# Kernel optimization log

Hardware: AMD Instinct MI355X
Metric: run time of the kernel (lower is better)

## Reference

```python
import jax, jax.numpy as jnp
import numpy as np

B, T, D = 2, 2048, 2048
N, KH, H = 16, 8, 128  # query heads, kv heads, head_dim
S = 2048               # cache size
EPS = 1e-6
ROPE_THETA = 1000000.0
K_MASK = -0.7 * float(np.finfo(np.float32).max)  # jax _get_large_negative(float32)


def _rms_norm(x, w):
    rms = jnp.sqrt(jnp.mean(x.astype(jnp.float32) ** 2, axis=-1, keepdims=True) + EPS)
    return (w * x / rms).astype(x.dtype)


def _rope_embeddings(positions, head_dim):
    fraction = jnp.arange(0, head_dim, 2, dtype=jnp.float32) / head_dim
    inv_freq = 1.0 / (ROPE_THETA ** fraction)
    sinusoid = jnp.einsum('BT,k->BTk', positions.astype(jnp.float32), inv_freq,
                          precision=jax.lax.Precision.HIGHEST)
    return jnp.sin(sinusoid), jnp.cos(sinusoid)


def _apply_rope(x, sin, cos):
    h = x.shape[-1] // 2
    x1, x2 = x[..., :h], x[..., h:]
    s, c = sin[:, :, None, :], cos[:, :, None, :]
    return jnp.concatenate([x1 * c - x2 * s, x2 * c + x1 * s], axis=-1).astype(x.dtype)


def _positions_from_segment_ids(seg):
    t = seg.shape[1]
    pos = jnp.arange(t, dtype=jnp.int32)[None, :] - jnp.argmax(seg, axis=1)[:, None]
    return jnp.where(seg != 0, pos, 2 ** 30)


def _num_left_pad(seg):
    return jnp.sum(jnp.cumsum(seg != 0, axis=-1) == 0, axis=-1).astype(jnp.int32)


def _attention(x, q_w, k_w, v_w, o_w, q_norm_w, k_norm_w, k_cache, v_cache,
               segment_ids, start_ind, cur_ind):
    b, t, _ = x.shape
    s = k_cache.shape[1]
    n, kh, h = q_w.shape[1], k_w.shape[1], q_w.shape[2]

    q = _rms_norm(jnp.einsum('BTD,DNH->BTNH', x, q_w), q_norm_w)  # [B,T,N,H]
    k = _rms_norm(jnp.einsum('BSD,DKH->BSKH', x, k_w), k_norm_w)  # [B,T,K,H]
    v = jnp.einsum('BSD,DKH->BSKH', x, v_w)                       # [B,T,K,H]

    start = jnp.where(start_ind < 0, _num_left_pad(segment_ids), start_ind)
    pos = _positions_from_segment_ids(segment_ids) + cur_ind
    sin, cos = _rope_embeddings(pos, h)
    q = _apply_rope(q, sin, cos)
    k = _apply_rope(k, sin, cos)

    # KV-cache update at cur_ind
    k_cache = jax.lax.dynamic_update_slice(k_cache, k, (0, cur_ind, 0, 0))
    v_cache = jax.lax.dynamic_update_slice(v_cache, v, (0, cur_ind, 0, 0))

    # GQA: group query heads per kv head
    qg = q.reshape(b, t, kh, n // kh, h)
    logits = jnp.einsum('BTHGD,BSHD->BHGTS', qg, k_cache) * (h ** -0.5)

    q_pos = cur_ind + jnp.arange(t, dtype=jnp.int32)[None, :] - start[:, None]  # [B,T]
    ts = jnp.arange(s, dtype=jnp.int32)
    kv_seg = (ts[None, :] >= start[:, None]) & (ts[None, :] < cur_ind + t)      # [B,S] bool
    k_pos = ts[None, :] - start[:, None]                                        # [B,S]
    causal = k_pos[:, None, :] <= q_pos[:, :, None]                             # [B,T,S]
    # faithful to original: bool kv segment ids compared against int segment_ids
    seg_mask = kv_seg[:, None, :].astype(segment_ids.dtype) == segment_ids[:, :, None]
    final_mask = (causal & seg_mask)[:, None, None, :, :]                       # [B,1,1,T,S]

    logits = jnp.where(final_mask, logits, K_MASK)
    attn = jax.nn.softmax(logits.astype(jnp.float32), axis=-1).astype(logits.dtype)
    o = jnp.einsum('BHGTS,BSHD->BTHGD', attn, v_cache).reshape(b, t, n, h)
    return jnp.einsum('BTNH,NHD->BTD', o, o_w)


def setup_inputs() -> dict:
    key = jax.random.key(0)
    ks = jax.random.split(key, 5)
    scale = 0.02
    return {
        'x': jax.random.normal(ks[0], (B, T, D), jnp.float32),
        'q_w': jax.random.normal(ks[1], (D, N, H), jnp.float32) * scale,
        'k_w': jax.random.normal(ks[2], (D, KH, H), jnp.float32) * scale,
        'v_w': jax.random.normal(ks[3], (D, KH, H), jnp.float32) * scale,
        'o_w': jax.random.normal(ks[4], (N, H, D), jnp.float32) * scale,
        'q_norm_w': jnp.ones((H,), jnp.float32),
        'k_norm_w': jnp.ones((H,), jnp.float32),
        'k_cache': jnp.zeros((B, S, KH, H), jnp.float32),
        'v_cache': jnp.zeros((B, S, KH, H), jnp.float32),
        'segment_ids': jnp.ones((B, T), jnp.int32),
        'start_ind': jnp.zeros((B,), jnp.int32),
        'cur_ind': 0,
        'right_pads': 0,
    }


def reference(x, q_w, k_w, v_w, o_w, q_norm_w, k_norm_w, k_cache, v_cache,
              segment_ids, start_ind, cur_ind, right_pads):
    # right_pads only advances the cache write pointer (stateful side effect); it
    # does not affect the attention output.
    return _attention(x, q_w, k_w, v_w, o_w, q_norm_w, k_norm_w,
                      k_cache, v_cache, segment_ids, start_ind, cur_ind)
```

## Files before the change

kernel.cpp:

```cpp
#include <hip/hip_runtime.h>
#include <hip/hip_fp16.h>
#include <climits>
#include <math.h>

#define Bc   2
#define Tc   2048
#define Dc   2048
#define Nc   16
#define KHc  8
#define Hc   128
#define Sc   2048

constexpr float EPSc   = 1e-6f;
constexpr float SCALE2 = 0.1275174477984469f;

typedef short short8 __attribute__((ext_vector_type(8)));
typedef _Float16 half8 __attribute__((ext_vector_type(8)));
typedef __fp16 fp16x2 __attribute__((ext_vector_type(2)));
typedef float float4v __attribute__((ext_vector_type(4)));

union U16x8 { uint4 u; short8 s8; half8 h8; unsigned short us[8]; };
union H2U  { fp16x2 h; unsigned u; };
union S8H8 { short8 s; half8 h; };

__device__ __forceinline__ unsigned short f2bf(float f) {
    union { float f; unsigned u; } v; v.f = f;
    unsigned r = v.u + 0x7FFFu + ((v.u >> 16) & 1u);
    return (unsigned short)(r >> 16);
}
__device__ __forceinline__ float bf2f(unsigned short u) {
    union { unsigned u; float f; } v; v.u = ((unsigned)u) << 16;
    return v.f;
}

__device__ __forceinline__ void tc_body(const float* __restrict__ in,
                                        unsigned short* __restrict__ out,
                                        int R, int C, int bx, int by, int tid,
                                        float tile[32][33])
{
    int c0 = bx * 32, r0 = by * 32;
#pragma unroll
    for (int i = 0; i < 4; ++i) {
        int row = (tid >> 5) + i * 8, col = tid & 31;
        tile[row][col] = in[(size_t)(r0 + row) * C + c0 + col];
    }
    __syncthreads();
#pragma unroll
    for (int i = 0; i < 4; ++i) {
        int rowo = (tid >> 5) + i * 8, colo = tid & 31;
        out[(size_t)(c0 + rowo) * R + r0 + colo] = f2bf(tile[colo][rowo]);
    }
}

__global__ __launch_bounds__(256) void prep(const float* __restrict__ x,
                                            const float* __restrict__ qw,
                                            const float* __restrict__ kw,
                                            const float* __restrict__ vw,
                                            const float* __restrict__ ow,
                                            const int* __restrict__ seg,
                                            const int* __restrict__ start_ind,
                                            int* __restrict__ meta,
                                            unsigned short* __restrict__ xb,
                                            unsigned short* __restrict__ qkvwT,
                                            unsigned short* __restrict__ owT)
{
    __shared__ float tile[32][33];
    __shared__ int s_max, s_amax, s_nz;
    int id = blockIdx.x;
    int tid = threadIdx.x;

    if (id < Bc) {
        int b = id;
        if (tid == 0) { s_max = INT_MIN; s_amax = Tc; s_nz = Tc; }
        __syncthreads();
        int lmax = INT_MIN;
        for (int t = tid; t < Tc; t += 256) lmax = max(lmax, seg[b * Tc + t]);
        atomicMax(&s_max, lmax);
        __syncthreads();
        int mv = s_max;
        int lamax = Tc, lnz = Tc;
        for (int t = tid; t < Tc; t += 256) {
            int v = seg[b * Tc + t];
            if (v == mv) lamax = min(lamax, t);
            if (v != 0)  lnz   = min(lnz, t);
        }
        atomicMin(&s_amax, lamax);
        atomicMin(&s_nz, lnz);
        __syncthreads();
        if (tid == 0) {
            meta[b] = s_amax;
            int st = start_ind[b];
            meta[Bc + b] = (st < 0) ? s_nz : st;
        }
        return;
    }
    id -= Bc;
    if (id < 4096) {
        size_t base = ((size_t)id * 256 + tid) * 8;
        float4 a = *(const float4*)&x[base];
        float4 b = *(const float4*)&x[base + 4];
        U16x8 o;
        o.us[0] = f2bf(a.x); o.us[1] = f2bf(a.y); o.us[2] = f2bf(a.z); o.us[3] = f2bf(a.w);
        o.us[4] = f2bf(b.x); o.us[5] = f2bf(b.y); o.us[6] = f2bf(b.z); o.us[7] = f2bf(b.w);
        *(uint4*)&xb[base] = o.u;
        return;
    }
    id -= 4096;
    if (id < 4096) { tc_body(qw, qkvwT, 2048, 2048, id & 63, id >> 6, tid, tile); return; }
    id -= 4096;
    if (id < 2048) { tc_body(kw, qkvwT + (size_t)2048 * 2048, 2048, 1024, id & 31, id >> 5, tid, tile); return; }
    id -= 2048;
    if (id < 2048) { tc_body(vw, qkvwT + (size_t)3072 * 2048, 2048, 1024, id & 31, id >> 5, tid, tile); return; }
    id -= 2048;
    tc_body(ow, owT, 2048, 2048, id & 63, id >> 6, tid, tile);
}

__global__ __launch_bounds__(512, 2) void gemm256(const unsigned short* __restrict__ A,
                                                  const unsigned short* __restrict__ BT,
                                                  void* __restrict__ Cout,
                                                  int M, int N, int K, int out_fp32)
{
    __shared__ __align__(16) unsigned short As[2 * 16384];
    __shared__ __align__(16) unsigned short Bs[2 * 16384];

    int tid = threadIdx.x;
    int lane = tid & 63, w = tid >> 6;
    int quad = lane >> 4, l15 = lane & 15;

    int gx = gridDim.x;
    int nwg = gx * gridDim.y;
    int lin = blockIdx.y * gx + blockIdx.x;
    int swz = (lin & 7) * (nwg >> 3) + (lin >> 3);
    int bm = (swz / gx) * 256, bn = (swz % gx) * 256;

    int KT = K >> 6;

    int colswz = (((lane & 7) ^ ((lane >> 3) & 7)) << 3);
    int r0 = (w * 2) * 8 + (lane >> 3);
    int r1 = (w * 2 + 1) * 8 + (lane >> 3);
    const unsigned short* Ab0 = A + (size_t)(bm + r0) * K + colswz;
    const unsigned short* Ab1 = A + (size_t)(bm + r1) * K + colswz;
    const unsigned short* Bb0 = BT + (size_t)(bn + r0) * K + colswz;
    const unsigned short* Bb1 = BT + (size_t)(bn + r1) * K + colswz;
    size_t hK = (size_t)128 * K;

    unsigned short* dA0 = As + (w * 2) * 512;
    unsigned short* dA1 = As + (w * 2 + 1) * 512;
    unsigned short* dB0 = Bs + (w * 2) * 512;
    unsigned short* dB1 = Bs + (w * 2 + 1) * 512;

    auto stA = [&](int kt, int h, int bufp) __attribute__((always_inline)) {
        __builtin_amdgcn_global_load_lds(
            (__attribute__((address_space(1))) void*)(Ab0 + h * hK + (size_t)kt * 64),
            (__attribute__((address_space(3))) void*)(dA0 + bufp * 16384 + h * 8192), 16, 0, 0);
        __builtin_amdgcn_global_load_lds(
            (__attribute__((address_space(1))) void*)(Ab1 + h * hK + (size_t)kt * 64),
            (__attribute__((address_space(3))) void*)(dA1 + bufp * 16384 + h * 8192), 16, 0, 0);
    };
    auto stB = [&](int kt, int h, int bufp) __attribute__((always_inline)) {
        __builtin_amdgcn_global_load_lds(
            (__attribute__((address_space(1))) void*)(Bb0 + h * hK + (size_t)kt * 64),
            (__attribute__((address_space(3))) void*)(dB0 + bufp * 16384 + h * 8192), 16, 0, 0);
        __builtin_amdgcn_global_load_lds(
            (__attribute__((address_space(1))) void*)(Bb1 + h * hK + (size_t)kt * 64),
            (__attribute__((address_space(3))) void*)(dB1 + bufp * 16384 + h * 8192), 16, 0, 0);
    };

    int ards = (w >> 2) * 8192;
    int brds = (w & 3) * 4096;
    int rowb = l15 * 64;
    int swA = l15 & 7;
    int cof0 = ((quad) ^ swA) << 3;
    int cof1 = ((4 + quad) ^ swA) << 3;

    float4v acc[8][4];
#pragma unroll
    for (int i = 0; i < 8; ++i)
#pragma unroll
        for (int j = 0; j < 4; ++j) acc[i][j] = (float4v)0.f;

    stA(0, 0, 0); stA(0, 1, 0); stB(0, 0, 0); stB(0, 1, 0);
    stA(1, 0, 1); stA(1, 1, 1); stB(1, 0, 1); stB(1, 1, 1);
    asm volatile("s_waitcnt vmcnt(8)" ::: "memory");
    __builtin_amdgcn_s_barrier();
    asm volatile("" ::: "memory");

    auto ktile = [&](int kt, int bufp) __attribute__((always_inline)) {
        const unsigned short* ab = As + bufp * 16384 + ards + rowb;
        const unsigned short* bb = Bs + bufp * 16384 + brds + rowb;
        short8 afl[2][4], afh[2][4], bfa[2][2], bfb[2][2];

#pragma unroll
        for (int mi = 0; mi < 4; ++mi) {
            afl[0][mi] = *(const short8*)&ab[mi * 1024 + cof0];
            afl[1][mi] = *(const short8*)&ab[mi * 1024 + cof1];
        }
#pragma unroll
        for (int ni = 0; ni < 2; ++ni) {
            bfa[0][ni] = *(const short8*)&bb[ni * 1024 + cof0];
            bfa[1][ni] = *(const short8*)&bb[ni * 1024 + cof1];
        }
#pragma unroll
        for (int ni = 0; ni < 2; ++ni) {
            bfb[0][ni] = *(const short8*)&bb[(2 + ni) * 1024 + cof0];
            bfb[1][ni] = *(const short8*)&bb[(2 + ni) * 1024 + cof1];
        }
#pragma unroll
        for (int mi = 0; mi < 4; ++mi) {
            afh[0][mi] = *(const short8*)&ab[(4 + mi) * 1024 + cof0];
            afh[1][mi] = *(const short8*)&ab[(4 + mi) * 1024 + cof1];
        }
        __builtin_amdgcn_s_setprio(1);
#pragma unroll
        for (int kk = 0; kk < 2; ++kk)
#pragma unroll
            for (int mi = 0; mi < 4; ++mi)
#pragma unroll
                for (int ni = 0; ni < 2; ++ni)
                    acc[mi][ni] = __builtin_amdgcn_mfma_f32_16x16x32_bf16(afl[kk][mi], bfa[kk][ni], acc[mi][ni], 0, 0, 0);
#pragma unroll
        for (int kk = 0; kk < 2; ++kk)
#pragma unroll
            for (int mi = 0; mi < 4; ++mi)
#pragma unroll
                for (int ni = 0; ni < 2; ++ni)
                    acc[mi][2 + ni] = __builtin_amdgcn_mfma_f32_16x16x32_bf16(afl[kk][mi], bfb[kk][ni], acc[mi][2 + ni], 0, 0, 0);
        __builtin_amdgcn_s_setprio(0);
        asm volatile("s_waitcnt lgkmcnt(0)" ::: "memory");
        __builtin_amdgcn_sched_barrier(0);
        __builtin_amdgcn_s_barrier();
        asm volatile("" ::: "memory");

        bool sA = (kt + 2) < KT;
        if (sA) {
            stA(kt + 2, 0, bufp); stA(kt + 2, 1, bufp);
            stB(kt + 2, 0, bufp); stB(kt + 2, 1, bufp);
        }
        __builtin_amdgcn_s_setprio(1);
#pragma unroll
        for (int kk = 0; kk < 2; ++kk)
#pragma unroll
            for (int mi = 0; mi < 4; ++mi)
#pragma unroll
                for (int ni = 0; ni < 2; ++ni)
                    acc[4 + mi][ni] = __builtin_amdgcn_mfma_f32_16x16x32_bf16(afh[kk][mi], bfa[kk][ni], acc[4 + mi][ni], 0, 0, 0);
#pragma unroll
        for (int kk = 0; kk < 2; ++kk)
#pragma unroll
            for (int mi = 0; mi < 4; ++mi)
#pragma unroll
                for (int ni = 0; ni < 2; ++ni)
                    acc[4 + mi][2 + ni] = __builtin_amdgcn_mfma_f32_16x16x32_bf16(afh[kk][mi], bfb[kk][ni], acc[4 + mi][2 + ni], 0, 0, 0);
        __builtin_amdgcn_s_setprio(0);
        if (sA) asm volatile("s_waitcnt vmcnt(8)" ::: "memory");
        else    asm volatile("s_waitcnt vmcnt(0)" ::: "memory");
        __builtin_amdgcn_sched_barrier(0);
        __builtin_amdgcn_s_barrier();
        asm volatile("" ::: "memory");
    };

    for (int kt = 0; kt < KT; kt += 2) {
        ktile(kt, 0);
        ktile(kt + 1, 1);
    }

    int wm = (w >> 2) * 128, wn = (w & 3) * 64;
#pragma unroll
    for (int mi = 0; mi < 8; ++mi)
#pragma unroll
        for (int ni = 0; ni < 4; ++ni)
#pragma unroll
            for (int reg = 0; reg < 4; ++reg) {
                int row = bm + wm + mi * 16 + quad * 4 + reg;
                int col = bn + wn + ni * 16 + l15;
                float v = acc[mi][ni][reg];
                if (out_fp32) ((float*)Cout)[(size_t)row * N + col] = v;
                else ((unsigned short*)Cout)[(size_t)row * N + col] = f2bf(v);
            }
}

__global__ __launch_bounds__(256) void post(unsigned short* __restrict__ QKVh,
                                            unsigned short* __restrict__ Kall,
                                            unsigned short* __restrict__ Vt,
                                            const float* __restrict__ qw,
                                            const float* __restrict__ kw,
                                            const int* __restrict__ seg,
                                            const int* __restrict__ meta,
                                            const int* __restrict__ cur_ptr,
                                            const float* __restrict__ kc,
                                            const float* __restrict__ vc)
{
    int id = blockIdx.x;
    int tid = threadIdx.x;
    int cur = cur_ptr[0];

    if (id < 24576) {
        int rowid = id * 4 + (tid >> 6);
        int lane = tid & 63;
        int hh = rowid % 24;
        int bt = rowid / 24;
        int t = bt & (Tc - 1);
        int b = bt >> 11;

        const unsigned short* in;
        unsigned short* out;
        const float* wt;
        if (hh < 16) {
            unsigned short* p = QKVh + (size_t)bt * 4096 + hh * Hc;
            in = p; out = p; wt = qw;
        } else {
            int kh = hh - 16;
            in = QKVh + (size_t)bt * 4096 + 2048 + kh * Hc;
            out = Kall + (((size_t)b * Sc + cur + t) * KHc + kh) * Hc;
            wt = kw;
        }
        float v1 = bf2f(in[lane]), v2 = bf2f(in[lane + 64]);
        float ssq = v1 * v1 + v2 * v2;
#pragma unroll
        for (int off = 1; off < 64; off <<= 1) ssq += __shfl_xor(ssq, off);
        float rinv = rsqrtf(ssq * (1.0f / Hc) + EPSc);

        int sg = seg[bt];
        long long pos = (sg != 0) ? (long long)(t - meta[b]) : (long long)(1 << 30);
        float posf = (float)(pos + (long long)cur);
        float inv_freq = exp2f(-(float)lane * (19.931568569324174f / 64.0f));
        float s, c;
        sincosf(posf * inv_freq, &s, &c);

        float n1 = wt[lane] * v1 * rinv;
        float n2 = wt[lane + 64] * v2 * rinv;
        out[lane]      = f2bf(n1 * c - n2 * s);
        out[lane + 64] = f2bf(n2 * c + n1 * s);
        return;
    }
    id -= 24576;
    if (id < 2048) {
        size_t base = ((size_t)id * 256 + tid) * 8;
        int s = (int)((base >> 10) & (Sc - 1));
        if (s >= cur && s < cur + Tc) return;
        float4 a = *(const float4*)&kc[base];
        float4 b = *(const float4*)&kc[base + 4];
        U16x8 o;
        o.us[0] = f2bf(a.x); o.us[1] = f2bf(a.y); o.us[2] = f2bf(a.z); o.us[3] = f2bf(a.w);
        o.us[4] = f2bf(b.x); o.us[5] = f2bf(b.y); o.us[6] = f2bf(b.z); o.us[7] = f2bf(b.w);
        *(uint4*)&Kall[base] = o.u;
        return;
    }
    id -= 2048;
    {
        int gid = id * 256 + tid;
        int h  = gid & 127;
        int s8 = ((gid >> 7) & 255) * 8;
        int kh = (gid >> 15) & 7;
        int b  = gid >> 18;
        int curT = cur + Tc;
        unsigned short tmp[8];
#pragma unroll
        for (int e = 0; e < 8; ++e) {
            int s = s8 + e;
            float f;
            if (s >= cur && s < curT)
                f = bf2f(QKVh[(size_t)(b * Tc + (s - cur)) * 4096 + 3072 + kh * Hc + h]);
            else
                f = vc[((size_t)(b * Sc + s) * KHc + kh) * Hc + h];
            tmp[e] = __half_as_ushort(__float2half(f));
        }
        *(uint4*)&Vt[(((size_t)b * KHc + kh) * Hc + h) * Sc + s8] = *(uint4*)tmp;
    }
}

__global__ __launch_bounds__(512, 4) void flash_mfma(const unsigned short* __restrict__ Qb,
                                                     const unsigned short* __restrict__ Kall,
                                                     const unsigned short* __restrict__ Vt,
                                                     const int* __restrict__ seg,
                                                     const int* __restrict__ meta,
                                                     const int* __restrict__ cur_ptr,
                                                     unsigned short* __restrict__ Ob)
{
    __shared__ __align__(16) unsigned short Ks[64 * 128];
    __shared__ __align__(16) unsigned short Vs[128 * 64];
    __shared__ __align__(16) unsigned short Ps[128 * 64];

    int tid = threadIdx.x;
    int lane = tid & 63, w = tid >> 6;
    int quad = lane >> 4, l15 = lane & 15;
    int bid = blockIdx.x;
    int raw = bid & 15;
    int n  = (bid >> 4) & 15;
    int b  = bid >> 8;
    int qt = (b == 0) ? raw : (15 - raw);
    int kh = n >> 1;
    int cur = cur_ptr[0];
    int startb = meta[Bc + b];
    int curT = cur + Tc;
    int t0 = qt * 128 + w * 16;

    short8 qf[4];
#pragma unroll
    for (int ks = 0; ks < 4; ++ks) {
        int row = t0 + l15;
        U16x8 uq;
        uq.u = *(const uint4*)&Qb[(size_t)(b * Tc + row) * 4096 + n * Hc + ks * 32 + quad * 8];
        qf[ks] = uq.s8;
    }

    int trow0 = t0 + l15;
    int sg0 = seg[b * Tc + trow0];
    int cls = (sg0 == 0) ? 0 : ((sg0 == 1) ? 1 : 2);
    int ct  = cur + trow0;
    unsigned long long mball = __ballot(cls == 1);
    bool allseg1 = (mball == 0xFFFFFFFFFFFFFFFFull);

    float lsum = 0.f;
    float4v oT[8];
#pragma unroll
    for (int i = 0; i < 8; ++i) oT[i] = (float4v)0.f;

    int s_end = min(Sc, cur + qt * 128 + 128);
    int nch = (s_end + 63) >> 6;

    const size_t kstride = (size_t)KHc * Hc;
    const unsigned short* kptr[2];
    unsigned short* kdst[2];
#pragma unroll
    for (int i = 0; i < 2; ++i) {
        int j = w * 2 + i;
        int row = j * 4 + (lane >> 4);
        int pl = lane & 15;
        int pg = pl ^ ((row >> 1) & 7);
        kptr[i] = Kall + (size_t)b * Sc * kstride + (size_t)row * kstride + kh * Hc + pg * 8;
        kdst[i] = Ks + j * 512;
    }
    const unsigned short* vptr[2];
    unsigned short* vdst[2];
#pragma unroll
    for (int i = 0; i < 2; ++i) {
        int j = w * 2 + i;
        int h = j * 8 + (lane >> 3);
        int pl = lane & 7;
        int pg = pl ^ ((h >> 1) & 7);
        vptr[i] = Vt + ((size_t)b * KHc + kh) * (size_t)Hc * Sc + (size_t)h * Sc + pg * 8;
        vdst[i] = Vs + j * 512;
    }
    int sw3 = (l15 >> 1) & 7;
    int sw8 = l15 & 7;
    unsigned short* psrow = Ps + (w * 16 + l15) * 64;

    for (int c = 0; c < nch; ++c) {
        int s0 = c * 64;
#pragma unroll
        for (int i = 0; i < 2; ++i) {
            __builtin_amdgcn_global_load_lds(
                (__attribute__((address_space(1))) void*)(kptr[i] + (size_t)s0 * kstride),
                (__attribute__((address_space(3))) void*)kdst[i], 16, 0, 0);
            __builtin_amdgcn_global_load_lds(
                (__attribute__((address_space(1))) void*)(vptr[i] + s0),
                (__attribute__((address_space(3))) void*)vdst[i], 16, 0, 0);
        }
        __syncthreads();

        float4v st[4];
#pragma unroll
        for (int i = 0; i < 4; ++i) st[i] = (float4v)0.f;
        __builtin_amdgcn_s_setprio(1);
#pragma unroll
        for (int ks = 0; ks < 4; ++ks) {
#pragma unroll
            for (int stile = 0; stile < 4; ++stile) {
                short8 kf = *(const short8*)&Ks[(stile * 16 + l15) * 128 + ((ks * 4 + quad) ^ sw3) * 8];
                st[stile] = __builtin_amdgcn_mfma_f32_16x16x32_bf16(kf, qf[ks], st[stile], 0, 0, 0);
            }
        }
        __builtin_amdgcn_s_setprio(0);

        bool fullok = allseg1 && (s0 >= startb) && (s0 + 63 <= cur + t0) && (s0 + 63 < curT);

#pragma unroll
        for (int stile = 0; stile < 4; ++stile) {
            float p0, p1, p2, p3;
            if (fullok) {
                p0 = exp2f(st[stile][0] * SCALE2);
                p1 = exp2f(st[stile][1] * SCALE2);
                p2 = exp2f(st[stile][2] * SCALE2);
                p3 = exp2f(st[stile][3] * SCALE2);
            } else {
                float pp[4];
#pragma unroll
                for (int reg = 0; reg < 4; ++reg) {
                    int s = s0 + stile * 16 + quad * 4 + reg;
                    int kvseg = (s >= startb && s < curT) ? 1 : 0;
                    bool ok = (s <= ct) && (cls == kvseg);
                    pp[reg] = exp2f(ok ? st[stile][reg] * SCALE2 : -1e30f);
                }
                p0 = pp[0]; p1 = pp[1]; p2 = pp[2]; p3 = pp[3];
            }
            lsum += (p0 + p1) + (p2 + p3);
            H2U a, d;
            a.h = __builtin_amdgcn_cvt_pkrtz(p0, p1);
            d.h = __builtin_amdgcn_cvt_pkrtz(p2, p3);
            uint2 pk; pk.x = a.u; pk.y = d.u;
            *(uint2*)&psrow[(((stile * 2 + (quad >> 1)) ^ sw8) << 3) + (quad & 1) * 4] = pk;
        }

        __builtin_amdgcn_s_setprio(1);
#pragma unroll
        for (int kk = 0; kk < 2; ++kk) {
            S8H8 pf;
            pf.s = *(const short8*)&psrow[((kk * 4 + quad) ^ sw8) << 3];
#pragma unroll
            for (int htile = 0; htile < 8; ++htile) {
                S8H8 vf;
                vf.s = *(const short8*)&Vs[(htile * 16 + l15) * 64 + ((kk * 4 + quad) ^ sw3) * 8];
                oT[htile] = __builtin_amdgcn_mfma_f32_16x16x32_f16(vf.h, pf.h, oT[htile], 0, 0, 0);
            }
        }
        __builtin_amdgcn_s_setprio(0);

        __syncthreads();
    }

    float l = lsum;
    l += __shfl_xor(l, 16);
    l += __shfl_xor(l, 32);
    float linv = (l > 0.f) ? (1.0f / l) : 0.f;

    {
        int trow = t0 + l15;
        size_t base = ((size_t)(b * Tc + trow) * Nc + n) * Hc;
#pragma unroll
        for (int htile = 0; htile < 8; ++htile) {
            float4v v = oT[htile];
            unsigned short r0 = f2bf(v[0] * linv);
            unsigned short r1 = f2bf(v[1] * linv);
            unsigned short r2 = f2bf(v[2] * linv);
            unsigned short r3 = f2bf(v[3] * linv);
            uint2 pk;
            pk.x = (unsigned)r0 | ((unsigned)r1 << 16);
            pk.y = (unsigned)r2 | ((unsigned)r3 << 16);
            *(uint2*)&Ob[base + htile * 16 + quad * 4] = pk;
        }
    }
}

extern "C" void kernel_launch(void* const* d_in, const int* in_sizes, int n_in,
                              void* d_out, int out_size, void* d_ws, size_t ws_size,
                              hipStream_t stream)
{
    const float* x        = (const float*)d_in[0];
    const float* q_w      = (const float*)d_in[1];
    const float* k_w      = (const float*)d_in[2];
    const float* v_w      = (const float*)d_in[3];
    const float* o_w      = (const float*)d_in[4];
    const float* q_norm_w = (const float*)d_in[5];
    const float* k_norm_w = (const float*)d_in[6];
    const float* k_cache  = (const float*)d_in[7];
    const float* v_cache  = (const float*)d_in[8];
    const int*   seg      = (const int*)d_in[9];
    const int*   startind = (const int*)d_in[10];
    const int*   cur_ptr  = (const int*)d_in[11];
    (void)in_sizes; (void)n_in; (void)out_size; (void)ws_size;

    char* base = (char*)d_ws;
    int* meta = (int*)base;
    unsigned short* QKVh = (unsigned short*)(base + 1024);
    unsigned short* Kall = (unsigned short*)(base + 33555456);
    unsigned short* Vt   = (unsigned short*)(base + 41944064);
    unsigned short* xb   = (unsigned short*)(base + 50332672);
    unsigned short* qkvwT= (unsigned short*)(base + 67109888);
    unsigned short* owT  = (unsigned short*)(base + 83887104);
    unsigned short* Ob   = xb;

    prep<<<Bc + 4096 + 4096 + 2048 + 2048 + 4096, 256, 0, stream>>>(
        x, q_w, k_w, v_w, o_w, seg, startind, meta, xb, qkvwT, owT);

    gemm256<<<dim3(16, 16), 512, 0, stream>>>(xb, qkvwT, QKVh, Bc * Tc, 4096, Dc, 0);

    post<<<24576 + 2048 + 2048, 256, 0, stream>>>(QKVh, Kall, Vt,
        q_norm_w, k_norm_w, seg, meta, cur_ptr, k_cache, v_cache);

    flash_mfma<<<Bc * Nc * (Tc / 128), 512, 0, stream>>>(QKVh, Kall, Vt, seg, meta, cur_ptr, Ob);

    gemm256<<<dim3(8, 16), 512, 0, stream>>>(Ob, owT, d_out, Bc * Tc, Dc, Nc * Hc, 1);
}
```

Measured before the change: 457.8 us.

## Stagger A and B tile prefetch and interleave LDS reads with MFMA

```diff
diff --git a/kernel.cpp b/kernel.cpp
--- a/kernel.cpp
+++ b/kernel.cpp
@@ -137,33 +137,35 @@
 
     int colswz = (((lane & 7) ^ ((lane >> 3) & 7)) << 3);
     int r0 = (w * 2) * 8 + (lane >> 3);
-    int r1 = (w * 2 + 1) * 8 + (lane >> 3);
     const unsigned short* Ab0 = A + (size_t)(bm + r0) * K + colswz;
-    const unsigned short* Ab1 = A + (size_t)(bm + r1) * K + colswz;
     const unsigned short* Bb0 = BT + (size_t)(bn + r0) * K + colswz;
-    const unsigned short* Bb1 = BT + (size_t)(bn + r1) * K + colswz;
+    size_t rowK8 = (size_t)8 * K;
     size_t hK = (size_t)128 * K;
 
     unsigned short* dA0 = As + (w * 2) * 512;
-    unsigned short* dA1 = As + (w * 2 + 1) * 512;
     unsigned short* dB0 = Bs + (w * 2) * 512;
-    unsigned short* dB1 = Bs + (w * 2 + 1) * 512;
-
-    auto stA = [&](int kt, int h, int bufp) __attribute__((always_inline)) {
-        __builtin_amdgcn_global_load_lds(
-            (__attribute__((address_space(1))) void*)(Ab0 + h * hK + (size_t)kt * 64),
-            (__attribute__((address_space(3))) void*)(dA0 + bufp * 16384 + h * 8192), 16, 0, 0);
-        __builtin_amdgcn_global_load_lds(
-            (__attribute__((address_space(1))) void*)(Ab1 + h * hK + (size_t)kt * 64),
-            (__attribute__((address_space(3))) void*)(dA1 + bufp * 16384 + h * 8192), 16, 0, 0);
+
+    auto stA = [&](int kt, int bufp) __attribute__((always_inline)) {
+#pragma unroll
+        for (int h = 0; h < 2; ++h) {
+            __builtin_amdgcn_global_load_lds(
+                (__attribute__((address_space(1))) void*)(Ab0 + h * hK + (size_t)kt * 64),
+                (__attribute__((address_space(3))) void*)(dA0 + bufp * 16384 + h * 8192), 16, 0, 0);
+            __builtin_amdgcn_global_load_lds(
+                (__attribute__((address_space(1))) void*)(Ab0 + h * hK + rowK8 + (size_t)kt * 64),
+                (__attribute__((address_space(3))) void*)(dA0 + bufp * 16384 + h * 8192 + 512), 16, 0, 0);
+        }
     };
-    auto stB = [&](int kt, int h, int bufp) __attribute__((always_inline)) {
-        __builtin_amdgcn_global_load_lds(
-            (__attribute__((address_space(1))) void*)(Bb0 + h * hK + (size_t)kt * 64),
-            (__attribute__((address_space(3))) void*)(dB0 + bufp * 16384 + h * 8192), 16, 0, 0);
-        __builtin_amdgcn_global_load_lds(
-            (__attribute__((address_space(1))) void*)(Bb1 + h * hK + (size_t)kt * 64),
-            (__attribute__((address_space(3))) void*)(dB1 + bufp * 16384 + h * 8192), 16, 0, 0);
+    auto stB = [&](int kt, int bufp) __attribute__((always_inline)) {
+#pragma unroll
+        for (int h = 0; h < 2; ++h) {
+            __builtin_amdgcn_global_load_lds(
+                (__attribute__((address_space(1))) void*)(Bb0 + h * hK + (size_t)kt * 64),
+                (__attribute__((address_space(3))) void*)(dB0 + bufp * 16384 + h * 8192), 16, 0, 0);
+            __builtin_amdgcn_global_load_lds(
+                (__attribute__((address_space(1))) void*)(Bb0 + h * hK + rowK8 + (size_t)kt * 64),
+                (__attribute__((address_space(3))) void*)(dB0 + bufp * 16384 + h * 8192 + 512), 16, 0, 0);
+        }
     };
 
     int ards = (w >> 2) * 8192;
@@ -179,9 +181,9 @@
 #pragma unroll
         for (int j = 0; j < 4; ++j) acc[i][j] = (float4v)0.f;
 
-    stA(0, 0, 0); stA(0, 1, 0); stB(0, 0, 0); stB(0, 1, 0);
-    stA(1, 0, 1); stA(1, 1, 1); stB(1, 0, 1); stB(1, 1, 1);
-    asm volatile("s_waitcnt vmcnt(8)" ::: "memory");
+    stA(0, 0); stB(0, 0);
+    stA(1, 1);
+    asm volatile("s_waitcnt vmcnt(4)" ::: "memory");
     __builtin_amdgcn_s_barrier();
     asm volatile("" ::: "memory");
 
@@ -190,6 +192,7 @@
         const unsigned short* bb = Bs + bufp * 16384 + brds + rowb;
         short8 afl[2][4], afh[2][4], bfa[2][2], bfb[2][2];
 
+        if (kt + 1 < KT) stB(kt + 1, bufp ^ 1);
 #pragma unroll
         for (int mi = 0; mi < 4; ++mi) {
             afl[0][mi] = *(const short8*)&ab[mi * 1024 + cof0];
@@ -200,42 +203,41 @@
             bfa[0][ni] = *(const short8*)&bb[ni * 1024 + cof0];
             bfa[1][ni] = *(const short8*)&bb[ni * 1024 + cof1];
         }
+        __builtin_amdgcn_s_setprio(1);
+#pragma unroll
+        for (int kk = 0; kk < 2; ++kk)
+#pragma unroll
+            for (int mi = 0; mi < 4; ++mi)
+#pragma unroll
+                for (int ni = 0; ni < 2; ++ni)
+                    acc[mi][ni] = __builtin_amdgcn_mfma_f32_16x16x32_bf16(afl[kk][mi], bfa[kk][ni], acc[mi][ni], 0, 0, 0);
+        __builtin_amdgcn_s_setprio(0);
 #pragma unroll
         for (int ni = 0; ni < 2; ++ni) {
             bfb[0][ni] = *(const short8*)&bb[(2 + ni) * 1024 + cof0];
             bfb[1][ni] = *(const short8*)&bb[(2 + ni) * 1024 + cof1];
         }
+        __builtin_amdgcn_s_setprio(1);
+#pragma unroll
+        for (int kk = 0; kk < 2; ++kk)
+#pragma unroll
+            for (int mi = 0; mi < 4; ++mi)
+#pragma unroll
+                for (int ni = 0; ni < 2; ++ni)
+                    acc[mi][2 + ni] = __builtin_amdgcn_mfma_f32_16x16x32_bf16(afl[kk][mi], bfb[kk][ni], acc[mi][2 + ni], 0, 0, 0);
+        __builtin_amdgcn_s_setprio(0);
 #pragma unroll
         for (int mi = 0; mi < 4; ++mi) {
             afh[0][mi] = *(const short8*)&ab[(4 + mi) * 1024 + cof0];
             afh[1][mi] = *(const short8*)&ab[(4 + mi) * 1024 + cof1];
         }
-        __builtin_amdgcn_s_setprio(1);
-#pragma unroll
-        for (int kk = 0; kk < 2; ++kk)
-#pragma unroll
-            for (int mi = 0; mi < 4; ++mi)
-#pragma unroll
-                for (int ni = 0; ni < 2; ++ni)
-                    acc[mi][ni] = __builtin_amdgcn_mfma_f32_16x16x32_bf16(afl[kk][mi], bfa[kk][ni], acc[mi][ni], 0, 0, 0);
-#pragma unroll
-        for (int kk = 0; kk < 2; ++kk)
-#pragma unroll
-            for (int mi = 0; mi < 4; ++mi)
-#pragma unroll
-                for (int ni = 0; ni < 2; ++ni)
-                    acc[mi][2 + ni] = __builtin_amdgcn_mfma_f32_16x16x32_bf16(afl[kk][mi], bfb[kk][ni], acc[mi][2 + ni], 0, 0, 0);
-        __builtin_amdgcn_s_setprio(0);
         asm volatile("s_waitcnt lgkmcnt(0)" ::: "memory");
         __builtin_amdgcn_sched_barrier(0);
         __builtin_amdgcn_s_barrier();
         asm volatile("" ::: "memory");
 
         bool sA = (kt + 2) < KT;
-        if (sA) {
-            stA(kt + 2, 0, bufp); stA(kt + 2, 1, bufp);
-            stB(kt + 2, 0, bufp); stB(kt + 2, 1, bufp);
-        }
+        if (sA) stA(kt + 2, bufp);
         __builtin_amdgcn_s_setprio(1);
 #pragma unroll
         for (int kk = 0; kk < 2; ++kk)
@@ -252,7 +254,7 @@
                 for (int ni = 0; ni < 2; ++ni)
                     acc[4 + mi][2 + ni] = __builtin_amdgcn_mfma_f32_16x16x32_bf16(afh[kk][mi], bfb[kk][ni], acc[4 + mi][2 + ni], 0, 0, 0);
         __builtin_amdgcn_s_setprio(0);
-        if (sA) asm volatile("s_waitcnt vmcnt(8)" ::: "memory");
+        if (sA) asm volatile("s_waitcnt vmcnt(4)" ::: "memory");
         else    asm volatile("s_waitcnt vmcnt(0)" ::: "memory");
         __builtin_amdgcn_sched_barrier(0);
         __builtin_amdgcn_s_barrier();
```

Result: faster. 393.3 us (-14.1%).
